# Optimization experiments

Hardware: AMD Instinct MI355X
Metric: run time of the kernel (lower is better)

Reference implementation:

```python
import jax, jax.numpy as jnp
import numpy as np

N, D = 32768, 256   # tokens, latent dim
K = 4096            # codebook size


def setup_inputs() -> dict:
    key = jax.random.key(0)
    k1, k2 = jax.random.split(key)
    x = jax.random.normal(k1, (N, D), dtype=jnp.float32)
    embed = jax.random.normal(k2, (1, K, D), dtype=jnp.float32)
    return {"x": x, "embed": embed}


def reference(x, embed):
    # x: [N, D] -> ndim<4 branch adds leading dim; flatten = [1, N, D]
    x = x.astype(jnp.float32)
    f = x.reshape(-1, x.shape[-1])          # [N, D]  (flatten.squeeze(0))
    e = embed[0]                             # [K, D]  (embed.squeeze(0))
    # squared euclidean distance (== torch.cdist(...,p=2).pow(2))
    x_sq = jnp.sum(f * f, axis=-1, keepdims=True)        # [N, 1]
    e_sq = jnp.sum(e * e, axis=-1)                        # [K]
    dist = x_sq + e_sq[None, :] - 2.0 * (f @ e.T)         # [N, K]
    dist = jnp.maximum(dist, 0.0)[None]                   # [1, N, K]
    embed_ind = jnp.argmin(dist, axis=-1)                 # [1, N]
    # one-hot @ embed == embedding gather
    quantize = jnp.take(e, embed_ind[0], axis=0)          # [N, D]
    return quantize, embed_ind, dist
```

## Files before the change

### kernel.cpp

```cpp
#include <hip/hip_runtime.h>

#define NTOK 32768
#define DIM  256
#define KCB  4096
#define MARGIN 4.0f
#define CAP  24

typedef __attribute__((ext_vector_type(8))) short s8v;
typedef __attribute__((ext_vector_type(4))) float f32x4;

__device__ __forceinline__ unsigned short f2bf(float f) {
    union { float f; unsigned u; } v; v.f = f;
    unsigned r = v.u + 0x7FFFu + ((v.u >> 16) & 1u);
    return (unsigned short)(r >> 16);
}

__global__ __launch_bounds__(64)
void prep(const float* __restrict__ x, const float* __restrict__ e,
          unsigned short* __restrict__ eb, unsigned short* __restrict__ xb,
          float* __restrict__ esq, float* __restrict__ xsq)
{
    int j = blockIdx.x;
    int l = threadIdx.x;
    const float4* src; unsigned short* dstb; float* dsts; int row;
    if (j < KCB) { src = (const float4*)e; dstb = eb; dsts = esq; row = j; }
    else         { src = (const float4*)x; dstb = xb; dsts = xsq; row = j - KCB; }

    float4 v = src[(size_t)row * 64 + l];
    float s = v.x*v.x + v.y*v.y + v.z*v.z + v.w*v.w;
    #pragma unroll
    for (int m = 32; m >= 1; m >>= 1) s += __shfl_xor(s, m);
    if (l == 0) dsts[row] = s;

    int rb = row >> 4, lr = row & 15;
    int ks = l >> 3, g = (l >> 1) & 3;
    unsigned lo = (unsigned)f2bf(v.x) | ((unsigned)f2bf(v.y) << 16);
    unsigned hi = (unsigned)f2bf(v.z) | ((unsigned)f2bf(v.w) << 16);
    uint2 p; p.x = lo; p.y = hi;
    size_t eidx = (size_t)rb * 4096 + ks * 512 + (g * 16 + lr) * 8 + (l & 1) * 4;
    *(uint2*)(dstb + eidx) = p;
}


#define MFMAB(CB4, ACC) { \
    _Pragma("unroll") \
    for (int ks = 0; ks < 8; ++ks) { \
        int fsp = (CB4) * 8 + ks + 3; if (fsp > 511) fsp = 511; \
        const char* pa = ebb + ((fsp >> 3) * 32768 + (fsp & 7) * 1024); \
        b[(ks + 3) & 3][0] = *(const s8v*)(pa); \
        b[(ks + 3) & 3][1] = *(const s8v*)(pa + 8192); \
        b[(ks + 3) & 3][2] = *(const s8v*)(pa + 16384); \
        b[(ks + 3) & 3][3] = *(const s8v*)(pa + 24576); \
        _Pragma("unroll") \
        for (int fi = 0; fi < 2; ++fi) \
            _Pragma("unroll") \
            for (int fj = 0; fj < 4; ++fj) \
                ACC[fi][fj] = __builtin_amdgcn_mfma_f32_16x16x32_bf16( \
                    a[fi][ks], b[ks & 3][fj], \
                    ks ? ACC[fi][fj] : (f32x4){0.f, 0.f, 0.f, 0.f}, 0, 0, 0); \
    } }

#define EPI(CB4, ACC) { \
    int cbase = (CB4) * 64; \
    float eq0 = esq[cbase + lr], eq1 = esq[cbase + 16 + lr]; \
    float eq2 = esq[cbase + 32 + lr], eq3 = esq[cbase + 48 + lr]; \
    _Pragma("unroll") \
    for (int fi = 0; fi < 2; ++fi) { \
        _Pragma("unroll") \
        for (int rg = 0; rg < 4; ++rg) { \
            float xq = xr[fi][rg]; \
            float d0 = fmaxf(xq + eq0 - 2.f * ACC[fi][0][rg], 0.f); \
            float d1 = fmaxf(xq + eq1 - 2.f * ACC[fi][1][rg], 0.f); \
            float d2 = fmaxf(xq + eq2 - 2.f * ACC[fi][2][rg], 0.f); \
            float d3 = fmaxf(xq + eq3 - 2.f * ACC[fi][3][rg], 0.f); \
            size_t rbase = (size_t)(wg * 32 + fi * 16 + g * 4 + rg) * KCB + cbase; \
            outd[rbase + lr]      = d0; \
            outd[rbase + 16 + lr] = d1; \
            outd[rbase + 32 + lr] = d2; \
            outd[rbase + 48 + lr] = d3; \
            float m = fminf(fminf(d0, d1), fminf(d2, d3)); \
            m = fminf(m, __shfl_xor(m, 1)); m = fminf(m, __shfl_xor(m, 2)); \
            m = fminf(m, __shfl_xor(m, 4)); m = fminf(m, __shfl_xor(m, 8)); \
            float nm = fminf(runmin[fi][rg], m); runmin[fi][rg] = nm; \
            float thr = nm + MARGIN; \
            int rloc = fi * 16 + g * 4 + rg; \
            _Pragma("unroll") \
            for (int fj = 0; fj < 4; ++fj) { \
                float dv = (fj == 0) ? d0 : (fj == 1) ? d1 : (fj == 2) ? d2 : d3; \
                bool hit = dv <= thr; \
                unsigned long long mk = __ballot(hit); \
                if (mk) { \
                    unsigned m16 = (unsigned)(mk >> (g * 16)) & 0xffffu; \
                    int pos = cnt[fi][rg] + __popc(m16 & ((1u << lr) - 1u)); \
                    if (hit && pos < CAP) cand[widx][rloc][pos] = cbase + fj * 16 + lr; \
                    cnt[fi][rg] += __popc(m16); \
                } \
            } \
        } \
    } }

__global__ __launch_bounds__(256, 1)
void vq_main(const float* __restrict__ x, const float* __restrict__ e,
             const unsigned short* __restrict__ eb, const unsigned short* __restrict__ xb,
             const float* __restrict__ esq, const float* __restrict__ xsq,
             float* __restrict__ outq, float* __restrict__ outi, float* __restrict__ outd)
{
    __shared__ int cand[4][32][CAP];
    __shared__ int cntL[4][32];

    const int tid = threadIdx.x;
    const int widx = tid >> 6;
    const int l = tid & 63;
    const int lr = l & 15;
    const int g = l >> 4;
    const int wg = blockIdx.x * 4 + widx;

    const char* xbb = (const char*)xb;
    s8v a[2][8];
    #pragma unroll
    for (int fi = 0; fi < 2; ++fi)
        #pragma unroll
        for (int ks = 0; ks < 8; ++ks)
            a[fi][ks] = *(const s8v*)(xbb +
                ((((size_t)(wg * 2 + fi) * 8 + ks) * 64 + l) << 4));

    float xr[2][4];
    #pragma unroll
    for (int fi = 0; fi < 2; ++fi)
        #pragma unroll
        for (int rg = 0; rg < 4; ++rg)
            xr[fi][rg] = xsq[wg * 32 + fi * 16 + g * 4 + rg];

    float runmin[2][4];
    int cnt[2][4];
    #pragma unroll
    for (int fi = 0; fi < 2; ++fi)
        #pragma unroll
        for (int rg = 0; rg < 4; ++rg) { runmin[fi][rg] = 1e30f; cnt[fi][rg] = 0; }

    f32x4 accA[2][4], accB[2][4];
    s8v b[4][4];
    const char* ebb = (const char*)eb + (l << 4);

    #pragma unroll
    for (int fs = 0; fs < 3; ++fs) {
        const char* pa = ebb + fs * 1024;
        b[fs][0] = *(const s8v*)(pa);
        b[fs][1] = *(const s8v*)(pa + 8192);
        b[fs][2] = *(const s8v*)(pa + 16384);
        b[fs][3] = *(const s8v*)(pa + 24576);
    }

    MFMAB(0, accA);
    #pragma unroll 1
    for (int cb2 = 0; cb2 < 31; ++cb2) {
        MFMAB(2 * cb2 + 1, accB);
        EPI(2 * cb2, accA);
        MFMAB(2 * cb2 + 2, accA);
        EPI(2 * cb2 + 1, accB);
    }
    MFMAB(63, accB);
    EPI(62, accA);
    EPI(63, accB);

    if (lr == 0) {
        #pragma unroll
        for (int fi = 0; fi < 2; ++fi)
            #pragma unroll
            for (int rg = 0; rg < 4; ++rg)
                cntL[widx][fi * 16 + g * 4 + rg] = cnt[fi][rg] < CAP ? cnt[fi][rg] : CAP;
    }
    __syncthreads();

    const float4* xf4 = (const float4*)x;
    const float4* ef4 = (const float4*)e;
    float4* qf4 = (float4*)outq;
    for (int rw = 0; rw < 32; ++rw) {
        int grow = wg * 32 + rw;
        int nc = cntL[widx][rw];
        float4 xv = xf4[(size_t)grow * 64 + l];
        double best = 1e300;
        int bestj = 0;
        for (int c = 0; c < nc; ++c) {
            int j = cand[widx][rw][c];
            float4 ev = ef4[(size_t)j * 64 + l];
            double dx = (double)xv.x - (double)ev.x; double s = dx * dx;
            double dy = (double)xv.y - (double)ev.y; s += dy * dy;
            double dz = (double)xv.z - (double)ev.z; s += dz * dz;
            double dw = (double)xv.w - (double)ev.w; s += dw * dw;
            #pragma unroll
            for (int m = 32; m >= 1; m >>= 1) s += __shfl_xor(s, m);
            if (s < best || (s == best && j < bestj)) { best = s; bestj = j; }
        }
        if (l == 0) outi[grow] = (float)bestj;
        float4 q = ef4[(size_t)bestj * 64 + l];
        qf4[(size_t)grow * 64 + l] = q;
    }
}

extern "C" void kernel_launch(void* const* d_in, const int* in_sizes, int n_in,
                              void* d_out, int out_size, void* d_ws, size_t ws_size,
                              hipStream_t stream) {
    const float* x = (const float*)d_in[0];
    const float* e = (const float*)d_in[1];
    char* ws = (char*)d_ws;
    unsigned short* eb  = (unsigned short*)ws;
    unsigned short* xb  = (unsigned short*)(ws + (size_t)2 * 1024 * 1024);
    float* esq = (float*)(ws + (size_t)18 * 1024 * 1024);
    float* xsq = esq + KCB;

    float* outq = (float*)d_out;
    float* outi = outq + (size_t)NTOK * DIM;
    float* outd = outi + NTOK;

    prep<<<dim3(NTOK + KCB), dim3(64), 0, stream>>>(x, e, eb, xb, esq, xsq);
    vq_main<<<dim3(256), dim3(256), 0, stream>>>(x, e, eb, xb, esq, xsq,
                                                 outq, outi, outd);
}
```

Baseline: 876.0 us.

## Halve rows per wave, double grid, stage esq in LDS, nontemporal output stores

Each wave now handles 16 token rows instead of 32, which halves the A fragments and accumulators held in registers. The grid doubles to 512 blocks and launch bounds allow 2 blocks per CU, raising occupancy. The codebook norms are staged once per block in shared memory, and the distance, index and quantize outputs use nontemporal stores. In exchange, each block streams the whole bf16 codebook for half as many rows, so codebook traffic per row doubles.

```diff
diff --git a/kernel.cpp b/kernel.cpp
--- a/kernel.cpp
+++ b/kernel.cpp
@@ -52,61 +52,57 @@
         b[(ks + 3) & 3][2] = *(const s8v*)(pa + 16384); \
         b[(ks + 3) & 3][3] = *(const s8v*)(pa + 24576); \
         _Pragma("unroll") \
-        for (int fi = 0; fi < 2; ++fi) \
-            _Pragma("unroll") \
-            for (int fj = 0; fj < 4; ++fj) \
-                ACC[fi][fj] = __builtin_amdgcn_mfma_f32_16x16x32_bf16( \
-                    a[fi][ks], b[ks & 3][fj], \
-                    ks ? ACC[fi][fj] : (f32x4){0.f, 0.f, 0.f, 0.f}, 0, 0, 0); \
+        for (int fj = 0; fj < 4; ++fj) \
+            ACC[fj] = __builtin_amdgcn_mfma_f32_16x16x32_bf16( \
+                a[ks], b[ks & 3][fj], \
+                ks ? ACC[fj] : (f32x4){0.f, 0.f, 0.f, 0.f}, 0, 0, 0); \
     } }
 
 #define EPI(CB4, ACC) { \
     int cbase = (CB4) * 64; \
-    float eq0 = esq[cbase + lr], eq1 = esq[cbase + 16 + lr]; \
-    float eq2 = esq[cbase + 32 + lr], eq3 = esq[cbase + 48 + lr]; \
+    float eq0 = esqL[cbase + lr], eq1 = esqL[cbase + 16 + lr]; \
+    float eq2 = esqL[cbase + 32 + lr], eq3 = esqL[cbase + 48 + lr]; \
     _Pragma("unroll") \
-    for (int fi = 0; fi < 2; ++fi) { \
+    for (int rg = 0; rg < 4; ++rg) { \
+        float xq = xr[rg]; \
+        float d0 = fmaxf(xq + eq0 - 2.f * ACC[0][rg], 0.f); \
+        float d1 = fmaxf(xq + eq1 - 2.f * ACC[1][rg], 0.f); \
+        float d2 = fmaxf(xq + eq2 - 2.f * ACC[2][rg], 0.f); \
+        float d3 = fmaxf(xq + eq3 - 2.f * ACC[3][rg], 0.f); \
+        size_t rbase = (size_t)(wg * 16 + g * 4 + rg) * KCB + cbase; \
+        __builtin_nontemporal_store(d0, &outd[rbase + lr]); \
+        __builtin_nontemporal_store(d1, &outd[rbase + 16 + lr]); \
+        __builtin_nontemporal_store(d2, &outd[rbase + 32 + lr]); \
+        __builtin_nontemporal_store(d3, &outd[rbase + 48 + lr]); \
+        float m = fminf(fminf(d0, d1), fminf(d2, d3)); \
+        m = fminf(m, __shfl_xor(m, 1)); m = fminf(m, __shfl_xor(m, 2)); \
+        m = fminf(m, __shfl_xor(m, 4)); m = fminf(m, __shfl_xor(m, 8)); \
+        float nm = fminf(runmin[rg], m); runmin[rg] = nm; \
+        float thr = nm + MARGIN; \
+        int rloc = g * 4 + rg; \
         _Pragma("unroll") \
-        for (int rg = 0; rg < 4; ++rg) { \
-            float xq = xr[fi][rg]; \
-            float d0 = fmaxf(xq + eq0 - 2.f * ACC[fi][0][rg], 0.f); \
-            float d1 = fmaxf(xq + eq1 - 2.f * ACC[fi][1][rg], 0.f); \
-            float d2 = fmaxf(xq + eq2 - 2.f * ACC[fi][2][rg], 0.f); \
-            float d3 = fmaxf(xq + eq3 - 2.f * ACC[fi][3][rg], 0.f); \
-            size_t rbase = (size_t)(wg * 32 + fi * 16 + g * 4 + rg) * KCB + cbase; \
-            outd[rbase + lr]      = d0; \
-            outd[rbase + 16 + lr] = d1; \
-            outd[rbase + 32 + lr] = d2; \
-            outd[rbase + 48 + lr] = d3; \
-            float m = fminf(fminf(d0, d1), fminf(d2, d3)); \
-            m = fminf(m, __shfl_xor(m, 1)); m = fminf(m, __shfl_xor(m, 2)); \
-            m = fminf(m, __shfl_xor(m, 4)); m = fminf(m, __shfl_xor(m, 8)); \
-            float nm = fminf(runmin[fi][rg], m); runmin[fi][rg] = nm; \
-            float thr = nm + MARGIN; \
-            int rloc = fi * 16 + g * 4 + rg; \
-            _Pragma("unroll") \
-            for (int fj = 0; fj < 4; ++fj) { \
-                float dv = (fj == 0) ? d0 : (fj == 1) ? d1 : (fj == 2) ? d2 : d3; \
-                bool hit = dv <= thr; \
-                unsigned long long mk = __ballot(hit); \
-                if (mk) { \
-                    unsigned m16 = (unsigned)(mk >> (g * 16)) & 0xffffu; \
-                    int pos = cnt[fi][rg] + __popc(m16 & ((1u << lr) - 1u)); \
-                    if (hit && pos < CAP) cand[widx][rloc][pos] = cbase + fj * 16 + lr; \
-                    cnt[fi][rg] += __popc(m16); \
-                } \
+        for (int fj = 0; fj < 4; ++fj) { \
+            float dv = (fj == 0) ? d0 : (fj == 1) ? d1 : (fj == 2) ? d2 : d3; \
+            bool hit = dv <= thr; \
+            unsigned long long mk = __ballot(hit); \
+            if (mk) { \
+                unsigned m16 = (unsigned)(mk >> (g * 16)) & 0xffffu; \
+                int pos = cnt[rg] + __popc(m16 & ((1u << lr) - 1u)); \
+                if (hit && pos < CAP) cand[widx][rloc][pos] = cbase + fj * 16 + lr; \
+                cnt[rg] += __popc(m16); \
             } \
         } \
     } }
 
-__global__ __launch_bounds__(256, 1)
+__global__ __launch_bounds__(256, 2)
 void vq_main(const float* __restrict__ x, const float* __restrict__ e,
              const unsigned short* __restrict__ eb, const unsigned short* __restrict__ xb,
              const float* __restrict__ esq, const float* __restrict__ xsq,
              float* __restrict__ outq, float* __restrict__ outi, float* __restrict__ outd)
 {
-    __shared__ int cand[4][32][CAP];
-    __shared__ int cntL[4][32];
+    __shared__ float esqL[KCB];
+    __shared__ int cand[4][16][CAP];
+    __shared__ int cntL[4][16];
 
     const int tid = threadIdx.x;
     const int widx = tid >> 6;
@@ -115,30 +111,27 @@
     const int g = l >> 4;
     const int wg = blockIdx.x * 4 + widx;
 
+    #pragma unroll
+    for (int i = 0; i < KCB / 256; ++i)
+        esqL[tid + i * 256] = esq[tid + i * 256];
+
     const char* xbb = (const char*)xb;
-    s8v a[2][8];
-    #pragma unroll
-    for (int fi = 0; fi < 2; ++fi)
-        #pragma unroll
-        for (int ks = 0; ks < 8; ++ks)
-            a[fi][ks] = *(const s8v*)(xbb +
-                ((((size_t)(wg * 2 + fi) * 8 + ks) * 64 + l) << 4));
-
-    float xr[2][4];
-    #pragma unroll
-    for (int fi = 0; fi < 2; ++fi)
-        #pragma unroll
-        for (int rg = 0; rg < 4; ++rg)
-            xr[fi][rg] = xsq[wg * 32 + fi * 16 + g * 4 + rg];
-
-    float runmin[2][4];
-    int cnt[2][4];
-    #pragma unroll
-    for (int fi = 0; fi < 2; ++fi)
-        #pragma unroll
-        for (int rg = 0; rg < 4; ++rg) { runmin[fi][rg] = 1e30f; cnt[fi][rg] = 0; }
-
-    f32x4 accA[2][4], accB[2][4];
+    s8v a[8];
+    #pragma unroll
+    for (int ks = 0; ks < 8; ++ks)
+        a[ks] = *(const s8v*)(xbb + ((((size_t)wg * 8 + ks) * 64 + l) << 4));
+
+    float xr[4];
+    #pragma unroll
+    for (int rg = 0; rg < 4; ++rg)
+        xr[rg] = xsq[wg * 16 + g * 4 + rg];
+
+    float runmin[4];
+    int cnt[4];
+    #pragma unroll
+    for (int rg = 0; rg < 4; ++rg) { runmin[rg] = 1e30f; cnt[rg] = 0; }
+
+    f32x4 accA[4], accB[4];
     s8v b[4][4];
     const char* ebb = (const char*)eb + (l << 4);
 
@@ -150,6 +143,8 @@
         b[fs][2] = *(const s8v*)(pa + 16384);
         b[fs][3] = *(const s8v*)(pa + 24576);
     }
+
+    __syncthreads();
 
     MFMAB(0, accA);
     #pragma unroll 1
@@ -165,18 +160,16 @@
 
     if (lr == 0) {
         #pragma unroll
-        for (int fi = 0; fi < 2; ++fi)
-            #pragma unroll
-            for (int rg = 0; rg < 4; ++rg)
-                cntL[widx][fi * 16 + g * 4 + rg] = cnt[fi][rg] < CAP ? cnt[fi][rg] : CAP;
+        for (int rg = 0; rg < 4; ++rg)
+            cntL[widx][g * 4 + rg] = cnt[rg] < CAP ? cnt[rg] : CAP;
     }
     __syncthreads();
 
     const float4* xf4 = (const float4*)x;
     const float4* ef4 = (const float4*)e;
-    float4* qf4 = (float4*)outq;
-    for (int rw = 0; rw < 32; ++rw) {
-        int grow = wg * 32 + rw;
+    f32x4* qf4 = (f32x4*)outq;
+    for (int rw = 0; rw < 16; ++rw) {
+        int grow = wg * 16 + rw;
         int nc = cntL[widx][rw];
         float4 xv = xf4[(size_t)grow * 64 + l];
         double best = 1e300;
@@ -192,9 +185,10 @@
             for (int m = 32; m >= 1; m >>= 1) s += __shfl_xor(s, m);
             if (s < best || (s == best && j < bestj)) { best = s; bestj = j; }
         }
-        if (l == 0) outi[grow] = (float)bestj;
+        if (l == 0) __builtin_nontemporal_store((float)bestj, &outi[grow]);
         float4 q = ef4[(size_t)bestj * 64 + l];
-        qf4[(size_t)grow * 64 + l] = q;
+        f32x4 qv = {q.x, q.y, q.z, q.w};
+        __builtin_nontemporal_store(qv, &qf4[(size_t)grow * 64 + l]);
     }
 }
 
@@ -214,6 +208,6 @@
     float* outd = outi + NTOK;
 
     prep<<<dim3(NTOK + KCB), dim3(64), 0, stream>>>(x, e, eb, xb, esq, xsq);
-    vq_main<<<dim3(256), dim3(256), 0, stream>>>(x, e, eb, xb, esq, xsq,
+    vq_main<<<dim3(512), dim3(256), 0, stream>>>(x, e, eb, xb, esq, xsq,
                                                  outq, outi, outd);
 }
```

New measurement: 730.5 us. 16.6% less time.
